# Kernel optimization log

Hardware: AMD Instinct MI355X
Metric: run time of the kernel (lower is better)

Reference implementation:

```python
import functools
import jax, jax.numpy as jnp
import numpy as np


def _peak_sums(x, R):
    """Vectorized Center_point_mapping.

    x: [N, C, H, W]; uses last channel as heatmap. A pixel (i,j) with
    1<=i<=H-2, 1<=j<=W-2 is a peak iff it is STRICTLY greater than all 8
    neighbors. Returns per-batch (sum of R*i, sum of R*j) over peaks [N,2]
    and per-batch peak counts [N].
    """
    h = x[:, -1]                       # [N, H, W]
    N, H, W = h.shape
    c = h[:, 1:-1, 1:-1]               # interior centers [N, H-2, W-2]
    neigh = (h[:, :-2, :-2], h[:, :-2, 1:-1], h[:, :-2, 2:],
             h[:, 1:-1, :-2],                  h[:, 1:-1, 2:],
             h[:, 2:, :-2],  h[:, 2:, 1:-1],  h[:, 2:, 2:])
    mask = functools.reduce(jnp.logical_and, (c > nb for nb in neigh))
    mf = mask.astype(jnp.float32)      # [N, H-2, W-2]
    iy = jnp.arange(1, H - 1, dtype=jnp.float32)
    ix = jnp.arange(1, W - 1, dtype=jnp.float32)
    sum_y = R * jnp.einsum('nij,i->n', mf, iy)   # sum of R*i per batch
    sum_x = R * jnp.einsum('nij,j->n', mf, ix)   # sum of R*j per batch
    count = jnp.sum(mf, axis=(1, 2))
    return jnp.stack([sum_y, sum_x], axis=-1), count


def _smooth_l1_sum(a, b):
    d = jnp.abs(a - b)
    return jnp.sum(jnp.where(d < 1.0, 0.5 * d * d, d - 0.5))


def setup_inputs() -> dict:
    key = jax.random.key(0)
    k1, k2, k3, k4 = jax.random.split(key, 4)
    N = 64
    p1 = jax.random.normal(k1, (N, 3, 256, 256), dtype=jnp.float32)
    p2 = jax.random.normal(k2, (N, 3, 128, 128), dtype=jnp.float32)
    p3 = jax.random.normal(k3, (N, 3, 64, 64), dtype=jnp.float32)
    target = jax.random.uniform(k4, (N, 32, 5), dtype=jnp.float32)
    return {"p1": p1, "p2": p2, "p3": p3, "target": target}


def reference(p1, p2, p3, target):
    s1, n1 = _peak_sums(p1, 4)
    s2, n2 = _peak_sums(p2, 8)
    s3, n3 = _peak_sums(p3, 16)
    center_sum = s1 + s2 + s3                 # [N, 2] per-batch coord sums
    point_sum = jnp.sum(n1 + n2 + n3)         # total peak count (scalar)
    center_sum_t = jnp.sum(center_sum, axis=0)

    boxes = target[:, :, :-1]                  # [N, num_obj, 4]
    centers = (boxes[:, :, 2:] + boxes[:, :, :2]) * 0.5   # [N, num_obj, 2]
    truths_sum = jnp.sum(centers, axis=1)      # [N, 2]
    truths_sum_t = jnp.sum(truths_sum, axis=0)

    off_x = _smooth_l1_sum(center_sum[:, 0], truths_sum[:, 0])
    off_y = _smooth_l1_sum(center_sum[:, 1], truths_sum[:, 1])
    loss = (off_x / jnp.abs(off_x) * (center_sum_t[0] - truths_sum_t[0])
            + off_y / jnp.abs(off_y) * (center_sum_t[1] - truths_sum_t[1])) / point_sum
    return loss
```

## Files before the change

kernel.cpp:

```cpp
#include <hip/hip_runtime.h>

#define G1 64
#define G2 32
#define G3 16
#define TT1 (G1*G1)
#define TT2 (G2*G2)
#define TT3 (G3*G3)
#define NBLK 21
#define NBATCH 64
#define NPART (NBLK*NBATCH)

template<int W>
__device__ __forceinline__ void load_row(const float* __restrict__ h, int r,
                                         int j0, bool fullj, float a[8]) {
    const float* p = h + r * W + (j0 - 1);
    float4 lo = *(const float4*)p;
    a[0] = lo.x; a[1] = lo.y; a[2] = lo.z; a[3] = lo.w;
    float4 hi = make_float4(0.f, 0.f, 0.f, 0.f);
    if (fullj) hi = *(const float4*)(p + 4);
    a[4] = hi.x; a[5] = hi.y; a[6] = hi.z; a[7] = hi.w;
}

template<int W, int R>
__device__ __forceinline__ void do_tile(const float* __restrict__ h,
                                        int ty, int tx,
                                        int& sy, int& sx, int& cnt) {
    const int i0 = 1 + 4 * ty;
    const int j0 = 1 + 4 * tx;
    const int ilast = min(i0 + 3, W - 2);
    const bool fullj = (j0 + 3 <= W - 2);

    float a[6][8];
    #pragma unroll
    for (int rr = 0; rr < 6; rr++) {
        const int r = min(i0 - 1 + rr, ilast + 1);
        load_row<W>(h, r, j0, fullj, a[rr]);
    }

    #pragma unroll
    for (int k = 0; k < 4; k++) {
        const int i = i0 + k;
        if (i <= ilast) {
            const float* top = a[k];
            const float* mid = a[k + 1];
            const float* bot = a[k + 2];
            #pragma unroll
            for (int p = 0; p < 4; p++) {
                const float c = mid[p + 1];
                bool pk = (c > top[p]) & (c > top[p + 1]) & (c > top[p + 2])
                        & (c > mid[p]) & (c > mid[p + 2])
                        & (c > bot[p]) & (c > bot[p + 1]) & (c > bot[p + 2]);
                if (pk && (j0 + p <= W - 2)) {
                    sy += R * i; sx += R * (j0 + p); cnt++;
                }
            }
        }
    }
}

__device__ __forceinline__ int wave_reduce_i(int v) {
    #pragma unroll
    for (int o = 32; o > 0; o >>= 1) v += __shfl_down(v, o, 64);
    return v;
}

__global__ __launch_bounds__(256) void peaks_kernel(
    const float* __restrict__ p1, const float* __restrict__ p2,
    const float* __restrict__ p3, int* __restrict__ ws) {
    const int n   = blockIdx.y;
    const int bx  = blockIdx.x;
    const int pid = bx * 256 + threadIdx.x;

    int sy = 0, sx = 0, c = 0;
    if (pid < TT1) {
        do_tile<256, 4>(p1 + n * 196608 + 131072, pid >> 6, pid & 63, sy, sx, c);
    } else if (pid < TT1 + TT2) {
        const int q = pid - TT1;
        do_tile<128, 8>(p2 + n * 49152 + 32768, q >> 5, q & 31, sy, sx, c);
    } else {
        const int q = pid - (TT1 + TT2);
        do_tile<64, 16>(p3 + n * 12288 + 8192, q >> 4, q & 15, sy, sx, c);
    }

    sy = wave_reduce_i(sy);
    sx = wave_reduce_i(sx);
    c  = wave_reduce_i(c);

    __shared__ int smem[3][4];
    const int lane = threadIdx.x & 63, wid = threadIdx.x >> 6;
    if (lane == 0) { smem[0][wid] = sy; smem[1][wid] = sx; smem[2][wid] = c; }
    __syncthreads();
    if (threadIdx.x == 0) {
        const int slot = n * NBLK + bx;
        ws[slot]             = smem[0][0] + smem[0][1] + smem[0][2] + smem[0][3];
        ws[NPART + slot]     = smem[1][0] + smem[1][1] + smem[1][2] + smem[1][3];
        ws[2 * NPART + slot] = smem[2][0] + smem[2][1] + smem[2][2] + smem[2][3];
    }
}

__global__ __launch_bounds__(64) void finalize_kernel(
    const int* __restrict__ ws, const float* __restrict__ target,
    float* __restrict__ out) {
    const int n = threadIdx.x;

    int isy = 0, isx = 0, cnt = 0;
    #pragma unroll
    for (int b = 0; b < NBLK; b++) {
        const int slot = n * NBLK + b;
        isy += ws[slot];
        isx += ws[NPART + slot];
        cnt += ws[2 * NPART + slot];
    }
    const float csy = (float)isy;
    const float csx = (float)isx;

    float ty = 0.f, tx = 0.f;
    const float* t = target + n * 160;
    #pragma unroll 8
    for (int k = 0; k < 32; k++) {
        ty += (t[k * 5 + 2] + t[k * 5 + 0]) * 0.5f;
        tx += (t[k * 5 + 3] + t[k * 5 + 1]) * 0.5f;
    }

    float dy = fabsf(csy - ty);
    float dx = fabsf(csx - tx);
    double offx = (dy < 1.f) ? 0.5 * (double)dy * dy : (double)dy - 0.5;
    double offy = (dx < 1.f) ? 0.5 * (double)dx * dx : (double)dx - 0.5;

    double cy_t = csy, cx_t = csx, ty_t = ty, tx_t = tx, pcnt = cnt;

    #pragma unroll
    for (int o = 32; o > 0; o >>= 1) {
        offx += __shfl_down(offx, o, 64);
        offy += __shfl_down(offy, o, 64);
        cy_t += __shfl_down(cy_t, o, 64);
        cx_t += __shfl_down(cx_t, o, 64);
        ty_t += __shfl_down(ty_t, o, 64);
        tx_t += __shfl_down(tx_t, o, 64);
        pcnt += __shfl_down(pcnt, o, 64);
    }

    if (n == 0) {
        double sgnx = offx / fabs(offx);
        double sgny = offy / fabs(offy);
        double loss = (sgnx * (cy_t - ty_t) + sgny * (cx_t - tx_t)) / pcnt;
        out[0] = (float)loss;
    }
}

extern "C" void kernel_launch(void* const* d_in, const int* in_sizes, int n_in,
                              void* d_out, int out_size, void* d_ws, size_t ws_size,
                              hipStream_t stream) {
    const float* p1     = (const float*)d_in[0];
    const float* p2     = (const float*)d_in[1];
    const float* p3     = (const float*)d_in[2];
    const float* target = (const float*)d_in[3];
    float* out = (float*)d_out;
    int*   ws  = (int*)d_ws;

    dim3 grid(NBLK, NBATCH);
    peaks_kernel<<<grid, 256, 0, stream>>>(p1, p2, p3, ws);
    finalize_kernel<<<1, 64, 0, stream>>>(ws, target, out);
}
```

Baseline: 103.4 us.

## Give each thread an 8-row tile and use one-wave blocks without LDS reduction

Each thread now evaluates an 8x4 tile of interior pixels instead of 4x4. It loads 10 halo rows instead of 6, so redundant row reads per output drop and the total thread count halves. The peak kernel is relaunched as 2688 single-wave blocks of 64 threads, 42 per batch, with each wave writing its partial sums directly. This removes the shared-memory staging and __syncthreads. The finalize kernel is adjusted to sum 42 partials per batch. The trade-off is higher register pressure and less parallelism per batch.

Result: no change. 104.1 us (+0.7%).

```diff
diff --git a/kernel.cpp b/kernel.cpp
--- a/kernel.cpp
+++ b/kernel.cpp
@@ -1,14 +1,11 @@
 #include <hip/hip_runtime.h>
 
-#define G1 64
-#define G2 32
-#define G3 16
-#define TT1 (G1*G1)
-#define TT2 (G2*G2)
-#define TT3 (G3*G3)
-#define NBLK 21
-#define NBATCH 64
-#define NPART (NBLK*NBATCH)
+#define TPB   2688
+#define B1    2048
+#define B2    2560
+#define NWAVE (TPB)
+#define NPART 2688
+#define WPB   42
 
 template<int W>
 __device__ __forceinline__ void load_row(const float* __restrict__ h, int r,
@@ -25,20 +22,20 @@
 __device__ __forceinline__ void do_tile(const float* __restrict__ h,
                                         int ty, int tx,
                                         int& sy, int& sx, int& cnt) {
-    const int i0 = 1 + 4 * ty;
+    const int i0 = 1 + 8 * ty;
     const int j0 = 1 + 4 * tx;
-    const int ilast = min(i0 + 3, W - 2);
-    const bool fullj = (j0 + 3 <= W - 2);
+    const int ilast = min(i0 + 7, W - 2);
+    const bool fullj = (j0 + 6 <= W - 1);
 
-    float a[6][8];
+    float a[10][8];
     #pragma unroll
-    for (int rr = 0; rr < 6; rr++) {
+    for (int rr = 0; rr < 10; rr++) {
         const int r = min(i0 - 1 + rr, ilast + 1);
         load_row<W>(h, r, j0, fullj, a[rr]);
     }
 
     #pragma unroll
-    for (int k = 0; k < 4; k++) {
+    for (int k = 0; k < 8; k++) {
         const int i = i0 + k;
         if (i <= ilast) {
             const float* top = a[k];
@@ -64,37 +61,33 @@
     return v;
 }
 
-__global__ __launch_bounds__(256) void peaks_kernel(
+__global__ __launch_bounds__(64) void peaks_kernel(
     const float* __restrict__ p1, const float* __restrict__ p2,
     const float* __restrict__ p3, int* __restrict__ ws) {
-    const int n   = blockIdx.y;
-    const int bx  = blockIdx.x;
-    const int pid = bx * 256 + threadIdx.x;
+    const int tid = blockIdx.x * 64 + threadIdx.x;
+    const int n   = tid / TPB;
+    const int q   = tid - n * TPB;
 
     int sy = 0, sx = 0, c = 0;
-    if (pid < TT1) {
-        do_tile<256, 4>(p1 + n * 196608 + 131072, pid >> 6, pid & 63, sy, sx, c);
-    } else if (pid < TT1 + TT2) {
-        const int q = pid - TT1;
-        do_tile<128, 8>(p2 + n * 49152 + 32768, q >> 5, q & 31, sy, sx, c);
+    if (q < B1) {
+        do_tile<256, 4>(p1 + n * 196608 + 131072, q >> 6, q & 63, sy, sx, c);
+    } else if (q < B2) {
+        const int q2 = q - B1;
+        do_tile<128, 8>(p2 + n * 49152 + 32768, q2 >> 5, q2 & 31, sy, sx, c);
     } else {
-        const int q = pid - (TT1 + TT2);
-        do_tile<64, 16>(p3 + n * 12288 + 8192, q >> 4, q & 15, sy, sx, c);
+        const int q3 = q - B2;
+        do_tile<64, 16>(p3 + n * 12288 + 8192, q3 >> 4, q3 & 15, sy, sx, c);
     }
 
     sy = wave_reduce_i(sy);
     sx = wave_reduce_i(sx);
     c  = wave_reduce_i(c);
 
-    __shared__ int smem[3][4];
-    const int lane = threadIdx.x & 63, wid = threadIdx.x >> 6;
-    if (lane == 0) { smem[0][wid] = sy; smem[1][wid] = sx; smem[2][wid] = c; }
-    __syncthreads();
     if (threadIdx.x == 0) {
-        const int slot = n * NBLK + bx;
-        ws[slot]             = smem[0][0] + smem[0][1] + smem[0][2] + smem[0][3];
-        ws[NPART + slot]     = smem[1][0] + smem[1][1] + smem[1][2] + smem[1][3];
-        ws[2 * NPART + slot] = smem[2][0] + smem[2][1] + smem[2][2] + smem[2][3];
+        const int w = blockIdx.x;
+        ws[w]             = sy;
+        ws[NPART + w]     = sx;
+        ws[2 * NPART + w] = c;
     }
 }
 
@@ -105,8 +98,8 @@
 
     int isy = 0, isx = 0, cnt = 0;
     #pragma unroll
-    for (int b = 0; b < NBLK; b++) {
-        const int slot = n * NBLK + b;
+    for (int b = 0; b < WPB; b++) {
+        const int slot = n * WPB + b;
         isy += ws[slot];
         isx += ws[NPART + slot];
         cnt += ws[2 * NPART + slot];
@@ -158,7 +151,6 @@
     float* out = (float*)d_out;
     int*   ws  = (int*)d_ws;
 
-    dim3 grid(NBLK, NBATCH);
-    peaks_kernel<<<grid, 256, 0, stream>>>(p1, p2, p3, ws);
+    peaks_kernel<<<2688, 64, 0, stream>>>(p1, p2, p3, ws);
     finalize_kernel<<<1, 64, 0, stream>>>(ws, target, out);
 }
```
